# Kernel tuning notes

Hardware: AMD Instinct MI355X
Metric: run time of the kernel (lower is better)

Reference implementation:

```python
import jax, jax.numpy as jnp
import numpy as np

B, S, W = 16, 512, 5
H, E, V = 512, 256, 100000


def setup_inputs() -> dict:
    key = jax.random.key(0)
    ks = jax.random.split(key, 20)
    inp = {
        "hiddens": jax.random.normal(ks[0], (B, S, H), jnp.float32),
        "masks": jax.random.randint(ks[1], (B, S), 0, 2, jnp.int32),
        "begins": jax.random.randint(ks[2], (B, S, W), 0, V, jnp.int32),
        "begin_lens": jax.random.randint(ks[3], (B, S), 0, W + 1, jnp.int32),
        "middles": jax.random.randint(ks[4], (B, S, W), 0, V, jnp.int32),
        "middle_lens": jax.random.randint(ks[5], (B, S), 0, W + 1, jnp.int32),
        "ends": jax.random.randint(ks[6], (B, S, W), 0, V, jnp.int32),
        "end_lens": jax.random.randint(ks[7], (B, S), 0, W + 1, jnp.int32),
        # parameters
        "emb": jax.random.normal(ks[8], (V, E), jnp.float32) * 0.02,
        "W_hidden": jax.random.normal(ks[9], (H, 3 * H), jnp.float32) * (1.0 / np.sqrt(H)),
        "b_hidden": jnp.zeros((3 * H,), jnp.float32),
        "W_begin": jax.random.normal(ks[10], (E, 2 * H), jnp.float32) * (1.0 / np.sqrt(E)),
        "b_begin": jnp.zeros((2 * H,), jnp.float32),
        "W_middle": jax.random.normal(ks[11], (E, 2 * H), jnp.float32) * (1.0 / np.sqrt(E)),
        "b_middle": jnp.zeros((2 * H,), jnp.float32),
        "W_end": jax.random.normal(ks[12], (E, 2 * H), jnp.float32) * (1.0 / np.sqrt(E)),
        "b_end": jnp.zeros((2 * H,), jnp.float32),
        "W_gate": jax.random.normal(ks[13], (H, 9), jnp.float32) * (1.0 / np.sqrt(H)),
        "b_gate": jnp.zeros((9,), jnp.float32),
    }
    return inp


def _len_mask(lens, w):
    # True where the lattice candidate is valid (mimics _make_mask's 1s)
    return jnp.arange(w)[None, None, :] < lens[:, :, None]


def _gates(hiddens, masks, W_gate, b_gate):
    b, s, _ = hiddens.shape
    lmr = hiddens @ W_gate + b_gate                      # (B,S,9)
    left, mid, right = jnp.split(lmr, 3, axis=-1)        # each (B,S,3)
    g = jax.nn.sigmoid(left[:, :-2] + mid[:, 1:-1] + right[:, 2:])  # (B,S-2,3)
    ones = jnp.ones((b, 1), g.dtype)
    zeros = jnp.zeros((b, 1), g.dtype)
    begin_g = jnp.concatenate([ones, g[..., 0], ones], axis=1)
    mid_g = jnp.concatenate([zeros, g[..., 1], zeros], axis=1)
    end_g = jnp.concatenate([ones, g[..., 2], ones], axis=1)
    pad = masks == 0
    z = jnp.zeros((), g.dtype)
    return (jnp.where(pad, z, begin_g), jnp.where(pad, z, mid_g), jnp.where(pad, z, end_g))


def reference(hiddens, masks, begins, begin_lens, middles, middle_lens, ends, end_lens,
              emb, W_hidden, b_hidden, W_begin, b_begin, W_middle, b_middle,
              W_end, b_end, W_gate, b_gate):
    w = begins.shape[-1]
    begin_m = _len_mask(begin_lens, w)
    middle_m = _len_mask(middle_lens, w)
    end_m = _len_mask(end_lens, w)

    begin_kv = emb[begins] @ W_begin + b_begin           # (B,S,W,2H)
    middle_kv = emb[middles] @ W_middle + b_middle
    end_kv = emb[ends] @ W_end + b_end

    query, hidden_key, hidden_value = jnp.split(hiddens @ W_hidden + b_hidden, 3, axis=-1)
    bg, mg, eg = _gates(hiddens, masks, W_gate, b_gate)
    begin_kv = bg[:, :, None, None] * begin_kv
    middle_kv = mg[:, :, None, None] * middle_kv
    end_kv = eg[:, :, None, None] * end_kv

    kv = jnp.concatenate([begin_kv, middle_kv, end_kv], axis=-2)   # (B,S,3W,2H)
    h = hiddens.shape[-1]
    keys, values = jnp.split(kv, 2, axis=-1)
    keys = jnp.concatenate([hidden_key[:, :, None, :], keys], axis=-2)     # (B,S,1+3W,H)
    values = jnp.concatenate([hidden_value[:, :, None, :], values], axis=-2)

    # combined mask: True entries get -1e10 (faithful to masked_fill_(masks, -1e10))
    score_mask = jnp.concatenate(
        [(masks != 0)[:, :, None], begin_m, middle_m, end_m], axis=-1)     # (B,S,1+3W)

    scores = jnp.einsum("bsh,bskh->bsk", query, keys)
    scores = jnp.where(score_mask, jnp.asarray(-1e10, scores.dtype), scores)
    weights = jax.nn.softmax(scores, axis=-1)
    return jnp.einsum("bsk,bskh->bsh", weights, values)
```

## Files before the change

### kernel.cpp

```cpp
#include <hip/hip_runtime.h>
#include <cstdint>
#include <cstddef>


typedef unsigned short u16;
typedef _Float16 f16;
typedef __attribute__((ext_vector_type(8))) f16 f16x8;
typedef __attribute__((ext_vector_type(4))) float f32x4;

#define MROWS 8192
#define SS 512

static __device__ __forceinline__ u16 f2h(float x) {
  f16 h = (f16)x;
  return __builtin_bit_cast(u16, h);
}
static __device__ __forceinline__ float h2f(u16 h) {
  return (float)__builtin_bit_cast(f16, h);
}
static __device__ __forceinline__ float sigm(float x) { return 1.f / (1.f + __expf(-x)); }

static __device__ __forceinline__ void gl2lds(const u16* g, u16* l) {
  __builtin_amdgcn_global_load_lds(
      (const __attribute__((address_space(1))) unsigned int*)g,
      (__attribute__((address_space(3))) unsigned int*)l, 16, 0, 0);
}

__global__ __launch_bounds__(256) void prep_all(
    const float* __restrict__ X, const float* __restrict__ Wg,
    const float* __restrict__ bg, const float* __restrict__ Wh,
    const float* __restrict__ Wb, const float* __restrict__ Wm,
    const float* __restrict__ We, const float* __restrict__ bb,
    const float* __restrict__ bm, const float* __restrict__ be,
    const float* __restrict__ bh, const int* __restrict__ masks,
    u16* __restrict__ Xh, float* __restrict__ lmr, float* __restrict__ s0,
    u16* __restrict__ Breg, u16* __restrict__ Acat, u16* __restrict__ Whq,
    u16* __restrict__ WvT, float* __restrict__ bcat, float* __restrict__ u,
    float* __restrict__ cbuf, int* __restrict__ idx, int* __restrict__ perm,
    int* __restrict__ cnts) {
  __shared__ float shmem[4608];
#define TI(r, c) shmem[(r)*65 + (c)]
  const int b = blockIdx.x;
  const int t = threadIdx.x;
  if (b < 64) {
    int k0 = (b & 7) * 64;
    int n0 = (b >> 3) * 64;
#pragma unroll
    for (int i = 0; i < 16; i++) {
      int li = i * 256 + t; int r = li >> 6, c = li & 63;
      TI(r, c) = Wh[(size_t)(k0 + r) * 1536 + 1024 + n0 + c];
    }
    __syncthreads();
#pragma unroll
    for (int i = 0; i < 16; i++) {
      int li = i * 256 + t; int r = li >> 6, c = li & 63;
      Breg[(size_t)(512 + n0 + r) * 512 + k0 + c] = f2h(TI(c, r));
    }
  } else if (b < 128) {
#pragma unroll
    for (int i = 0; i < 4; i++) {
      int q4 = (b - 64) * 1024 + t * 4 + i;
      int k = q4 >> 7;
      int c4 = (q4 & 127) * 4;
      float4 vq = *(const float4*)(Wh + (size_t)k * 1536 + c4);
      float4 vk = *(const float4*)(Wh + (size_t)k * 1536 + 512 + c4);
      ushort4 qh, kh;
      qh.x = f2h(vq.x); qh.y = f2h(vq.y); qh.z = f2h(vq.z); qh.w = f2h(vq.w);
      kh.x = f2h(vk.x); kh.y = f2h(vk.y); kh.z = f2h(vk.z); kh.w = f2h(vk.w);
      size_t o = (size_t)k * 512 + c4;
      *(ushort4*)(Whq + o) = qh;
      *(ushort4*)(Acat + o) = kh;
    }
  } else if (b < 576) {
    int tid = (b - 128) * 256 + t;
    int n = tid >> 7;
    int kq = (tid & 127) * 4;
    float4 v;
    if (n < 768) {
      int ty = n >> 8, c = n & 255;
      const float* src = (ty == 0 ? Wb : ty == 1 ? Wm : We) + (size_t)c * 1024 + kq;
      v = *(const float4*)src;
    } else if (n < 771) {
      int ty = n - 768;
      const float* src = (ty == 0 ? bb : ty == 1 ? bm : be) + kq;
      v = *(const float4*)src;
    } else {
      v = make_float4(0.f, 0.f, 0.f, 0.f);
    }
    ushort4 h; h.x = f2h(v.x); h.y = f2h(v.y); h.z = f2h(v.z); h.w = f2h(v.w);
    ((ushort4*)(Acat + (size_t)512 * 512))[tid] = h;
  } else if (b < 672) {
    int idx2 = b - 576;
    int ty = idx2 >> 5;
    int rem = idx2 & 31;
    int c0 = (rem & 3) * 64;
    int n0 = (rem >> 2) * 64;
    const float* Wsrc = ty == 0 ? Wb : ty == 1 ? Wm : We;
#pragma unroll
    for (int i = 0; i < 16; i++) {
      int li = i * 256 + t; int r = li >> 6, c = li & 63;
      TI(r, c) = Wsrc[(size_t)(c0 + r) * 1024 + 512 + n0 + c];
    }
    __syncthreads();
#pragma unroll
    for (int i = 0; i < 16; i++) {
      int li = i * 256 + t; int r = li >> 6, c = li & 63;
      WvT[(size_t)(n0 + r) * 768 + ty * 256 + c0 + c] = f2h(TI(c, r));
    }
  } else if (b < 1028) {
    const int lane = t & 63;
    const int widx = (b - 672) * 4 + (t >> 6);
    const int c = lane * 8;
    if (widx < 896) {
      int n = widx;
      float acc = 0.f;
      if (n < 771) {
        const float* src;
        if (n < 768) {
          int ty = n >> 8, ce = n & 255;
          src = (ty == 0 ? Wb : ty == 1 ? Wm : We) + (size_t)ce * 1024 + c;
        } else {
          int ty = n - 768;
          src = (ty == 0 ? bb : ty == 1 ? bm : be) + c;
        }
        float4 a0 = *(const float4*)src;
        float4 a1 = *(const float4*)(src + 4);
        float4 b0 = *(const float4*)(bh + c);
        float4 b1 = *(const float4*)(bh + c + 4);
        acc = a0.x * b0.x + a0.y * b0.y + a0.z * b0.z + a0.w * b0.w +
              a1.x * b1.x + a1.y * b1.y + a1.z * b1.z + a1.w * b1.w;
      }
#pragma unroll
      for (int o = 32; o > 0; o >>= 1) acc += __shfl_xor(acc, o);
      if (lane == 0) bcat[512 + n] = acc;
    } else if (widx < 1408) {
      int k = widx - 896;
      const float* wr = Wh + (size_t)k * 1536;
      float4 a0 = *(const float4*)(wr + c);
      float4 a1 = *(const float4*)(wr + c + 4);
      float4 a2 = *(const float4*)(wr + 512 + c);
      float4 a3 = *(const float4*)(wr + 512 + c + 4);
      float4 b0 = *(const float4*)(bh + 512 + c);
      float4 b1 = *(const float4*)(bh + 512 + c + 4);
      float4 b2 = *(const float4*)(bh + c);
      float4 b3 = *(const float4*)(bh + c + 4);
      float acc = a0.x * b0.x + a0.y * b0.y + a0.z * b0.z + a0.w * b0.w +
                  a1.x * b1.x + a1.y * b1.y + a1.z * b1.z + a1.w * b1.w +
                  a2.x * b2.x + a2.y * b2.y + a2.z * b2.z + a2.w * b2.w +
                  a3.x * b3.x + a3.y * b3.y + a3.z * b3.z + a3.w * b3.w;
#pragma unroll
      for (int o = 32; o > 0; o >>= 1) acc += __shfl_xor(acc, o);
      if (lane == 0) u[k] = acc;
    } else if (widx == 1408) {
      float4 b0 = *(const float4*)(bh + c);
      float4 b1 = *(const float4*)(bh + c + 4);
      float4 b2 = *(const float4*)(bh + 512 + c);
      float4 b3 = *(const float4*)(bh + 512 + c + 4);
      float acc = b0.x * b2.x + b0.y * b2.y + b0.z * b2.z + b0.w * b2.w +
                  b1.x * b3.x + b1.y * b3.y + b1.z * b3.z + b1.w * b3.w;
#pragma unroll
      for (int o = 32; o > 0; o >>= 1) acc += __shfl_xor(acc, o);
      if (lane == 0) cbuf[0] = acc;
    } else if (widx < 1417) {
      int i = (widx - 1409) * 64 + lane;
      bcat[i] = bh[1024 + i];
    }
  } else if (b < 1540) {
    const int xb = b - 1028;
    if (xb < 32) s0[xb * 256 + t] = 0.f;
    for (int i = t; i < 4608; i += 256) shmem[i] = Wg[i];
    __syncthreads();
    const int lane = t & 63, wid = t >> 6;
#pragma unroll
    for (int it = 0; it < 4; it++) {
      int pos = xb * 16 + it * 4 + wid;
      const float* x = X + (size_t)pos * 512 + lane * 8;
      float4 x0 = *(const float4*)x;
      float4 x1 = *(const float4*)(x + 4);
      float xs[8] = {x0.x, x0.y, x0.z, x0.w, x1.x, x1.y, x1.z, x1.w};
      ushort4 h0, h1;
      h0.x = f2h(xs[0]); h0.y = f2h(xs[1]); h0.z = f2h(xs[2]); h0.w = f2h(xs[3]);
      h1.x = f2h(xs[4]); h1.y = f2h(xs[5]); h1.z = f2h(xs[6]); h1.w = f2h(xs[7]);
      ((ushort4*)Xh)[pos * 128 + lane * 2] = h0;
      ((ushort4*)Xh)[pos * 128 + lane * 2 + 1] = h1;
      float p[9];
#pragma unroll
      for (int c = 0; c < 9; c++) p[c] = 0.f;
      const float* wrow = shmem + (lane * 8) * 9;
#pragma unroll
      for (int j = 0; j < 8; j++)
#pragma unroll
        for (int c = 0; c < 9; c++) p[c] += xs[j] * wrow[j * 9 + c];
#pragma unroll
      for (int c = 0; c < 9; c++)
#pragma unroll
        for (int o = 32; o > 0; o >>= 1) p[c] += __shfl_xor(p[c], o);
      if (lane == 0) {
#pragma unroll
        for (int c = 0; c < 9; c++) lmr[(size_t)pos * 9 + c] = p[c] + bg[c];
      }
    }
  } else {
    const int lane = t & 63;
    const int pos = (b - 1540) * 256 + t;
    bool is0 = masks[pos] == 0;
    unsigned long long bal = __ballot(is0);
    unsigned long long below = (lane == 0) ? 0ull : (~0ull >> (64 - lane));
    int rank0 = __popcll(bal & below);
    int rank1 = __popcll((~bal) & below);
    int n0w = __popcll(bal);
    int base0 = 0, base1 = 0;
    if (lane == 0) {
      base0 = atomicAdd(&cnts[0], n0w);
      base1 = atomicAdd(&cnts[1], 64 - n0w);
    }
    base0 = __shfl(base0, 0);
    base1 = __shfl(base1, 0);
    int slot = is0 ? (base0 + rank0) : (8191 - (base1 + rank1));
    perm[pos] = slot;
    idx[slot] = pos;
  }
#undef TI
}

template <int MODE>
__global__ __launch_bounds__(256) void gemm_k(
    const u16* __restrict__ A, const u16* __restrict__ Bt,
    const float* __restrict__ ubias, const float* __restrict__ bcat,
    float* __restrict__ Cf, u16* __restrict__ Cb, int Kdim,
    const u16* __restrict__ Xh, float* __restrict__ s0c,
    const int* __restrict__ idx, const int* __restrict__ cnts,
    const float4* __restrict__ sc4, const u16* __restrict__ HPb,
    const float* __restrict__ bb, const float* __restrict__ bm,
    const float* __restrict__ be) {
  constexpr int BROWS = (MODE == 2) ? 64 : 128;
  constexpr int NT = (MODE == 2) ? 2 : 4;
  __shared__ __align__(16) u16 As[2 * 128 * 32];
  __shared__ __align__(16) u16 Bs[2 * BROWS * 32];

  const int t = threadIdx.x;
  const int lane = t & 63;
  const int wid = t >> 6;
  const int m0 = blockIdx.x * 128;
  const int n0 = blockIdx.y * BROWS;

  bool remap = false;
  if constexpr (MODE == 0) {
    const int cnt0 = cnts[0];
    if (blockIdx.y < 4) {
      if (m0 >= cnt0) return;
      remap = true;
    } else if (blockIdx.y >= 8) {
      if (m0 + 128 <= cnt0) return;
      remap = true;
    }
  }

  int ra0 = m0 + (t >> 2), ra1 = m0 + 64 + (t >> 2);
  if (MODE == 0 && remap) { ra0 = idx[ra0]; ra1 = idx[ra1]; }
  const int rb0 = n0 + (t >> 2), rb1 = n0 + 64 + (t >> 2);
  const int koff = (t & 3) * 8;
  const int lds0 = (t >> 2) * 32 + koff;
  const int lds1 = 2048 + lds0;

  const int wm = (wid & 1) * 64;
  const int wn = (wid >> 1) * (NT * 16);
  const int fr = lane & 15;
  const int kq = (lane >> 4) * 8;

  f32x4 acc[4][NT];
#pragma unroll
  for (int i = 0; i < 4; i++)
#pragma unroll
    for (int j = 0; j < NT; j++) acc[i][j] = (f32x4){0.f, 0.f, 0.f, 0.f};

  auto STAGE = [&](int kb, int buf) {
    gl2lds(&A[(size_t)ra0 * Kdim + kb], &As[buf * 4096 + lds0]);
    gl2lds(&A[(size_t)ra1 * Kdim + kb], &As[buf * 4096 + lds1]);
    gl2lds(&Bt[(size_t)rb0 * Kdim + kb], &Bs[buf * (BROWS * 32) + lds0]);
    if constexpr (BROWS == 128)
      gl2lds(&Bt[(size_t)rb1 * Kdim + kb], &Bs[buf * (BROWS * 32) + lds1]);
  };
  auto COMPUTE = [&](int buf) {
    f16x8 av[4], bv[NT];
#pragma unroll
    for (int i = 0; i < 4; i++)
      av[i] = *(const f16x8*)&As[buf * 4096 + (wm + i * 16 + fr) * 32 + kq];
#pragma unroll
    for (int j = 0; j < NT; j++)
      bv[j] = *(const f16x8*)&Bs[buf * (BROWS * 32) + (wn + j * 16 + fr) * 32 + kq];
#pragma unroll
    for (int mt = 0; mt < 4; mt++)
#pragma unroll
      for (int nt = 0; nt < NT; nt++)
        acc[mt][nt] = __builtin_amdgcn_mfma_f32_16x16x32_f16(
            av[mt], bv[nt], acc[mt][nt], 0, 0, 0);
  };

  STAGE(koff, 0);
  __syncthreads();
  const int nk = Kdim >> 5;
  int buf = 0;
  for (int ki = 0; ki < nk - 1; ++ki) {
    STAGE((ki + 1) * 32 + koff, buf ^ 1);
    COMPUTE(buf);
    __syncthreads();
    buf ^= 1;
  }
  COMPUTE(buf);

  const int r0 = (lane >> 4) * 4;
  if constexpr (MODE == 0) {
    if (blockIdx.y < 4) {
      float pl[4][4];
      int xrow[4][4];
#pragma unroll
      for (int mt = 0; mt < 4; mt++)
#pragma unroll
        for (int r = 0; r < 4; r++) {
          pl[mt][r] = 0.f;
          xrow[mt][r] = idx[m0 + wm + mt * 16 + r0 + r];
        }
#pragma unroll
      for (int mt = 0; mt < 4; mt++)
#pragma unroll
        for (int nt = 0; nt < 4; nt++) {
          int col = n0 + wn + nt * 16 + fr;
          float bv2 = ubias[col];
#pragma unroll
          for (int r = 0; r < 4; r++)
            pl[mt][r] += (acc[mt][nt][r] + bv2) *
                         h2f(Xh[(size_t)xrow[mt][r] * 512 + col]);
        }
#pragma unroll
      for (int mt = 0; mt < 4; mt++)
#pragma unroll
        for (int r = 0; r < 4; r++) {
          float p = pl[mt][r];
          p += __shfl_xor(p, 1);
          p += __shfl_xor(p, 2);
          p += __shfl_xor(p, 4);
          p += __shfl_xor(p, 8);
          if (fr == r) {
            int slot = m0 + wm + mt * 16 + r0 + r;
            atomicAdd(&s0c[slot], p);
          }
        }
      return;
    }
    if (blockIdx.y < 8) {
#pragma unroll
      for (int mt = 0; mt < 4; mt++)
#pragma unroll
        for (int nt = 0; nt < 4; nt++) {
          int col = n0 - 512 + wn + nt * 16 + fr;
          float bv2 = bcat[col];
#pragma unroll
          for (int r = 0; r < 4; r++) {
            int row = m0 + wm + mt * 16 + r0 + r;
            Cb[(size_t)row * 1408 + col] = f2h(acc[mt][nt][r] + bv2);
          }
        }
    } else {
#pragma unroll
      for (int mt = 0; mt < 4; mt++)
#pragma unroll
        for (int nt = 0; nt < 4; nt++) {
          int pcol = n0 - 1024 + wn + nt * 16 + fr;
          float bv2 = bcat[512 + pcol];
#pragma unroll
          for (int r = 0; r < 4; r++) {
            int slot = m0 + wm + mt * 16 + r0 + r;
            Cb[(size_t)slot * 1408 + 512 + pcol] = f2h(acc[mt][nt][r] + bv2);
          }
        }
    }
  } else if constexpr (MODE == 1) {
#pragma unroll
    for (int mt = 0; mt < 4; mt++)
#pragma unroll
      for (int nt = 0; nt < 4; nt++) {
        int col = n0 + wn + nt * 16 + fr;
#pragma unroll
        for (int r = 0; r < 4; r++) {
          int row = m0 + wm + mt * 16 + r0 + r;
          int orow = row < 512 ? row : row + 512;
          Cb[(size_t)orow * 512 + col] = f2h(acc[mt][nt][r]);
        }
      }
  } else {
#pragma unroll
    for (int mt = 0; mt < 4; mt++)
#pragma unroll
      for (int nt = 0; nt < NT; nt++) {
        int col = n0 + wn + nt * 16 + fr;
        float b0 = bb[512 + col];
        float b1 = bm[512 + col];
        float b2 = be[512 + col];
#pragma unroll
        for (int r = 0; r < 4; r++) {
          int row = m0 + wm + mt * 16 + r0 + r;
          float4 s = sc4[row];
          float hv = h2f(HPb[(size_t)row * 1408 + col]);
          Cf[(size_t)row * 512 + col] =
              s.x * hv + s.y * b0 + s.z * b1 + s.w * b2 + acc[mt][nt][r];
        }
      }
  }
}

__global__ __launch_bounds__(256) void attn_kernel(
    const int* __restrict__ masks, const int* __restrict__ begins,
    const int* __restrict__ blens, const int* __restrict__ middles,
    const int* __restrict__ mlens, const int* __restrict__ ends,
    const int* __restrict__ elens, const float* __restrict__ emb,
    const u16* __restrict__ HPb, const float* __restrict__ lmr,
    const float* __restrict__ s0buf, const float* __restrict__ cbuf,
    const int* __restrict__ perm, float4* __restrict__ sc4,
    u16* __restrict__ Ebar) {
  const int t = threadIdx.x;
  const int lane = t & 63;
  const int wid = t >> 6;
  const int pos = blockIdx.x * 4 + wid;
  const int mask = masks[pos];
  const int slot = perm[pos];
  u16* erow = Ebar + (size_t)pos * 768;

  int l0 = min(blens[pos], 5), l1 = min(mlens[pos], 5), l2 = min(elens[pos], 5);
  int nv = l0 + l1 + l2;

  if (mask == 0) {
    float s0 = s0buf[slot] + cbuf[0];
    int ninv = 15 - nv;
    float w0;
    if (ninv == 0) {
      w0 = 1.f;
    } else {
      float Mx = fmaxf(s0, 0.f);
      float e0 = __expf(s0 - Mx);
      w0 = e0 / (e0 + (float)ninv * __expf(-Mx));
    }
    if (lane == 0) sc4[pos] = make_float4(w0, 0.f, 0.f, 0.f);
    ushort4 zz; zz.x = zz.y = zz.z = zz.w = 0;
    *(ushort4*)(erow + 0 * 256 + lane * 4) = zz;
    *(ushort4*)(erow + 1 * 256 + lane * 4) = zz;
    *(ushort4*)(erow + 2 * 256 + lane * 4) = zz;
  } else {
    const int s = pos & (SS - 1);
    float g[3];
    if (s == 0 || s == SS - 1) {
      g[0] = 1.f; g[1] = 0.f; g[2] = 1.f;
    } else {
      const float* p0 = lmr + (size_t)(pos - 1) * 9;
      const float* p1 = lmr + (size_t)pos * 9;
      const float* p2 = lmr + (size_t)(pos + 1) * 9;
      g[0] = sigm(p0[0] + p1[3] + p2[6]);
      g[1] = sigm(p0[1] + p1[4] + p2[7]);
      g[2] = sigm(p0[2] + p1[5] + p2[8]);
    }
    const bool deg = (nv == 15);
    int l[3] = {l0, l1, l2};
    if (deg) { l[0] = 0; l[1] = 0; l[2] = 0; }

    float4 Pt[3];
    float qb[3];
    if (!deg) {
      const u16* prow = HPb + (size_t)slot * 1408 + 512;
#pragma unroll
      for (int ty = 0; ty < 3; ty++) {
        ushort4 pu = *(const ushort4*)(prow + ty * 256 + lane * 4);
        Pt[ty].x = h2f(pu.x); Pt[ty].y = h2f(pu.y);
        Pt[ty].z = h2f(pu.z); Pt[ty].w = h2f(pu.w);
        qb[ty] = h2f(prow[768 + ty]);
      }
    }
    const int* idxp[3];
    idxp[0] = begins + (size_t)pos * 5;
    idxp[1] = middles + (size_t)pos * 5;
    idxp[2] = ends + (size_t)pos * 5;

    float4 ev[3][5];
    float scv[3][5];
    float Mx = deg ? 0.f : -3.0e38f;
#pragma unroll
    for (int ty = 0; ty < 3; ty++) {
#pragma unroll
      for (int w = 0; w < 5; w++) {
        bool act = (w >= l[ty]);
        if (act) {
          ev[ty][w] = *(const float4*)(emb + (size_t)idxp[ty][w] * 256 + lane * 4);
          float sv = 0.f;
          if (!deg) {
            float4 e = ev[ty][w];
            float d = Pt[ty].x * e.x + Pt[ty].y * e.y + Pt[ty].z * e.z + Pt[ty].w * e.w;
#pragma unroll
            for (int o = 32; o > 0; o >>= 1) d += __shfl_xor(d, o);
            sv = g[ty] * (d + qb[ty]);
          }
          scv[ty][w] = sv;
          Mx = fmaxf(Mx, sv);
        }
      }
    }
    float wts0 = deg ? 1.f : 0.f;
    float zs = wts0;
    float wts[3][5];
#pragma unroll
    for (int ty = 0; ty < 3; ty++)
#pragma unroll
      for (int w = 0; w < 5; w++) {
        bool act = (w >= l[ty]);
        float wv = act ? __expf(scv[ty][w] - Mx) : 0.f;
        wts[ty][w] = wv;
        zs += wv;
      }
    float inv = 1.f / zs;
    float alpha[3];
#pragma unroll
    for (int ty = 0; ty < 3; ty++) {
      float ax = 0.f, ay = 0.f, az = 0.f, aw = 0.f, asum = 0.f;
#pragma unroll
      for (int w = 0; w < 5; w++) {
        if (w >= l[ty]) {
          float wk = wts[ty][w];
          asum += wk;
          ax += wk * ev[ty][w].x;
          ay += wk * ev[ty][w].y;
          az += wk * ev[ty][w].z;
          aw += wk * ev[ty][w].w;
        }
      }
      float sg = g[ty] * inv;
      alpha[ty] = sg * asum;
      ushort4 h;
      h.x = f2h(ax * sg); h.y = f2h(ay * sg); h.z = f2h(az * sg); h.w = f2h(aw * sg);
      *(ushort4*)(erow + ty * 256 + lane * 4) = h;
    }
    if (lane == 0) sc4[pos] = make_float4(wts0 * inv, alpha[0], alpha[1], alpha[2]);
  }
}

extern "C" void kernel_launch(void* const* d_in, const int* in_sizes, int n_in,
                              void* d_out, int out_size, void* d_ws, size_t ws_size,
                              hipStream_t stream) {
  const float* hiddens = (const float*)d_in[0];
  const int* masks = (const int*)d_in[1];
  const int* begins = (const int*)d_in[2];
  const int* blens = (const int*)d_in[3];
  const int* middles = (const int*)d_in[4];
  const int* mlens = (const int*)d_in[5];
  const int* ends = (const int*)d_in[6];
  const int* elens = (const int*)d_in[7];
  const float* emb = (const float*)d_in[8];
  const float* Wh = (const float*)d_in[9];
  const float* bh = (const float*)d_in[10];
  const float* Wb = (const float*)d_in[11];
  const float* bb = (const float*)d_in[12];
  const float* Wm = (const float*)d_in[13];
  const float* bm = (const float*)d_in[14];
  const float* We = (const float*)d_in[15];
  const float* be = (const float*)d_in[16];
  const float* Wg = (const float*)d_in[17];
  const float* bg = (const float*)d_in[18];
  float* out = (float*)d_out;

  char* ws = (char*)d_ws;
  size_t off = 0;
  auto alloc = [&](size_t bytes) -> char* {
    char* p = ws + off;
    off += (bytes + 255) & ~(size_t)255;
    return p;
  };
  u16* Xh = (u16*)alloc((size_t)8192 * 512 * 2);
  u16* Whq = (u16*)alloc((size_t)512 * 512 * 2);
  u16* Acat = (u16*)alloc((size_t)1408 * 512 * 2);
  u16* Breg = (u16*)alloc((size_t)1920 * 512 * 2);
  u16* WvT = (u16*)alloc((size_t)512 * 768 * 2);
  u16* HPb = (u16*)alloc((size_t)8192 * 1408 * 2);
  float* lmr = (float*)alloc((size_t)8192 * 9 * 4);
  float* s0c = (float*)alloc((size_t)8192 * 4);
  float* bcat = (float*)alloc((size_t)1408 * 4);
  float* u = (float*)alloc((size_t)512 * 4);
  float* cbuf = (float*)alloc((size_t)4);
  float* sc4 = (float*)alloc((size_t)8192 * 4 * 4);
  u16* Ebar = (u16*)alloc((size_t)8192 * 768 * 2);
  int* idx = (int*)alloc((size_t)8192 * 4);
  int* perm = (int*)alloc((size_t)8192 * 4);
  int* cnts = (int*)alloc((size_t)256);
  if (off > ws_size) return;

  hipMemsetAsync(cnts, 0, 8, stream);
  prep_all<<<1572, 256, 0, stream>>>(hiddens, Wg, bg, Wh, Wb, Wm, We, bb, bm, be,
                                     bh, masks, Xh, lmr, s0c, Breg, Acat, Whq,
                                     WvT, bcat, u, cbuf, idx, perm, cnts);
  gemm_k<1><<<dim3(11, 4), 256, 0, stream>>>(
      Acat, Whq, nullptr, nullptr, nullptr, Breg, 512, nullptr, nullptr,
      nullptr, nullptr, nullptr, nullptr, nullptr, nullptr, nullptr);
  gemm_k<0><<<dim3(64, 15), 256, 0, stream>>>(
      Xh, Breg, u, bcat, nullptr, HPb, 512, Xh, s0c, idx, cnts,
      nullptr, nullptr, nullptr, nullptr, nullptr);
  attn_kernel<<<2048, 256, 0, stream>>>(masks, begins, blens, middles, mlens,
                                        ends, elens, emb, HPb, lmr, s0c, cbuf,
                                        perm, (float4*)sc4, Ebar);
  gemm_k<2><<<dim3(64, 8), 256, 0, stream>>>(
      Ebar, WvT, nullptr, nullptr, out, nullptr, 768, nullptr, nullptr,
      nullptr, nullptr, (const float4*)sc4, HPb, bb, bm, be);
}
```

Measured before the change: 287.7 us.

## Fuse weight-product GEMM into prep kernel, reading fp32 weights directly

```diff
diff --git a/kernel.cpp b/kernel.cpp
--- a/kernel.cpp
+++ b/kernel.cpp
@@ -34,11 +34,13 @@
     const float* __restrict__ bm, const float* __restrict__ be,
     const float* __restrict__ bh, const int* __restrict__ masks,
     u16* __restrict__ Xh, float* __restrict__ lmr, float* __restrict__ s0,
-    u16* __restrict__ Breg, u16* __restrict__ Acat, u16* __restrict__ Whq,
-    u16* __restrict__ WvT, float* __restrict__ bcat, float* __restrict__ u,
-    float* __restrict__ cbuf, int* __restrict__ idx, int* __restrict__ perm,
-    int* __restrict__ cnts) {
-  __shared__ float shmem[4608];
+    u16* __restrict__ Breg, u16* __restrict__ WvT, float* __restrict__ bcat,
+    float* __restrict__ u, float* __restrict__ cbuf, int* __restrict__ idx,
+    int* __restrict__ perm, int* __restrict__ cnts) {
+  __shared__ __align__(16) char smem_raw[32768];
+  float* shmem = (float*)smem_raw;
+  u16* As = (u16*)smem_raw;
+  u16* Bs = (u16*)(smem_raw + 16384);
 #define TI(r, c) shmem[(r)*65 + (c)]
   const int b = blockIdx.x;
   const int t = threadIdx.x;
@@ -56,41 +58,8 @@
       int li = i * 256 + t; int r = li >> 6, c = li & 63;
       Breg[(size_t)(512 + n0 + r) * 512 + k0 + c] = f2h(TI(c, r));
     }
-  } else if (b < 128) {
-#pragma unroll
-    for (int i = 0; i < 4; i++) {
-      int q4 = (b - 64) * 1024 + t * 4 + i;
-      int k = q4 >> 7;
-      int c4 = (q4 & 127) * 4;
-      float4 vq = *(const float4*)(Wh + (size_t)k * 1536 + c4);
-      float4 vk = *(const float4*)(Wh + (size_t)k * 1536 + 512 + c4);
-      ushort4 qh, kh;
-      qh.x = f2h(vq.x); qh.y = f2h(vq.y); qh.z = f2h(vq.z); qh.w = f2h(vq.w);
-      kh.x = f2h(vk.x); kh.y = f2h(vk.y); kh.z = f2h(vk.z); kh.w = f2h(vk.w);
-      size_t o = (size_t)k * 512 + c4;
-      *(ushort4*)(Whq + o) = qh;
-      *(ushort4*)(Acat + o) = kh;
-    }
-  } else if (b < 576) {
-    int tid = (b - 128) * 256 + t;
-    int n = tid >> 7;
-    int kq = (tid & 127) * 4;
-    float4 v;
-    if (n < 768) {
-      int ty = n >> 8, c = n & 255;
-      const float* src = (ty == 0 ? Wb : ty == 1 ? Wm : We) + (size_t)c * 1024 + kq;
-      v = *(const float4*)src;
-    } else if (n < 771) {
-      int ty = n - 768;
-      const float* src = (ty == 0 ? bb : ty == 1 ? bm : be) + kq;
-      v = *(const float4*)src;
-    } else {
-      v = make_float4(0.f, 0.f, 0.f, 0.f);
-    }
-    ushort4 h; h.x = f2h(v.x); h.y = f2h(v.y); h.z = f2h(v.z); h.w = f2h(v.w);
-    ((ushort4*)(Acat + (size_t)512 * 512))[tid] = h;
-  } else if (b < 672) {
-    int idx2 = b - 576;
+  } else if (b < 160) {
+    int idx2 = b - 64;
     int ty = idx2 >> 5;
     int rem = idx2 & 31;
     int c0 = (rem & 3) * 64;
@@ -107,9 +76,9 @@
       int li = i * 256 + t; int r = li >> 6, c = li & 63;
       WvT[(size_t)(n0 + r) * 768 + ty * 256 + c0 + c] = f2h(TI(c, r));
     }
-  } else if (b < 1028) {
+  } else if (b < 516) {
     const int lane = t & 63;
-    const int widx = (b - 672) * 4 + (t >> 6);
+    const int widx = (b - 160) * 4 + (t >> 6);
     const int c = lane * 8;
     if (widx < 896) {
       int n = widx;
@@ -165,8 +134,8 @@
       int i = (widx - 1409) * 64 + lane;
       bcat[i] = bh[1024 + i];
     }
-  } else if (b < 1540) {
-    const int xb = b - 1028;
+  } else if (b < 1028) {
+    const int xb = b - 516;
     if (xb < 32) s0[xb * 256 + t] = 0.f;
     for (int i = t; i < 4608; i += 256) shmem[i] = Wg[i];
     __syncthreads();
@@ -200,9 +169,9 @@
         for (int c = 0; c < 9; c++) lmr[(size_t)pos * 9 + c] = p[c] + bg[c];
       }
     }
-  } else {
+  } else if (b < 1060) {
     const int lane = t & 63;
-    const int pos = (b - 1540) * 256 + t;
+    const int pos = (b - 1028) * 256 + t;
     bool is0 = masks[pos] == 0;
     unsigned long long bal = __ballot(is0);
     unsigned long long below = (lane == 0) ? 0ull : (~0ull >> (64 - lane));
@@ -219,6 +188,96 @@
     int slot = is0 ? (base0 + rank0) : (8191 - (base1 + rank1));
     perm[pos] = slot;
     idx[slot] = pos;
+  } else {
+    const int b2 = b - 1060;
+    const int m0 = (b2 % 11) * 128;
+    const int n0 = (b2 / 11) * 128;
+    const int lane = t & 63;
+    const int wid = t >> 6;
+    const int row = t >> 2;
+    const int koff = (t & 3) * 8;
+    const int lds0 = row * 32 + koff;
+    const int lds1 = 2048 + lds0;
+
+    auto asrc = [&](int r) -> const float* {
+      if (r < 512) return Wh + (size_t)r * 1536 + 512;
+      int n = r - 512;
+      if (n < 768)
+        return (n < 256 ? Wb : n < 512 ? Wm : We) + (size_t)(n & 255) * 1024;
+      if (n < 771) return (n == 768 ? bb : n == 769 ? bm : be);
+      return nullptr;
+    };
+    const float* pa0 = asrc(m0 + row);
+    const float* pa1 = asrc(m0 + 64 + row);
+    const float* pb0 = Wh + (size_t)(n0 + row) * 1536;
+    const float* pb1 = Wh + (size_t)(n0 + 64 + row) * 1536;
+
+    const int wm = (wid & 1) * 64;
+    const int wn = (wid >> 1) * 64;
+    const int fr = lane & 15;
+    const int kq = (lane >> 4) * 8;
+
+    f32x4 acc[4][4];
+#pragma unroll
+    for (int i = 0; i < 4; i++)
+#pragma unroll
+      for (int j = 0; j < 4; j++) acc[i][j] = (f32x4){0.f, 0.f, 0.f, 0.f};
+
+    auto cvt8 = [&](const float* p, int col) -> f16x8 {
+      f16x8 h{};
+      if (p) {
+        float4 v0 = *(const float4*)(p + col);
+        float4 v1 = *(const float4*)(p + col + 4);
+        h[0] = (f16)v0.x; h[1] = (f16)v0.y; h[2] = (f16)v0.z; h[3] = (f16)v0.w;
+        h[4] = (f16)v1.x; h[5] = (f16)v1.y; h[6] = (f16)v1.z; h[7] = (f16)v1.w;
+      }
+      return h;
+    };
+    auto STAGE = [&](int kb, int buf) {
+      *(f16x8*)&As[buf * 4096 + lds0] = cvt8(pa0, kb + koff);
+      *(f16x8*)&As[buf * 4096 + lds1] = cvt8(pa1, kb + koff);
+      *(f16x8*)&Bs[buf * 4096 + lds0] = cvt8(pb0, kb + koff);
+      *(f16x8*)&Bs[buf * 4096 + lds1] = cvt8(pb1, kb + koff);
+    };
+    auto COMPUTE = [&](int buf) {
+      f16x8 av[4], bv[4];
+#pragma unroll
+      for (int i = 0; i < 4; i++) {
+        av[i] = *(const f16x8*)&As[buf * 4096 + (wm + i * 16 + fr) * 32 + kq];
+        bv[i] = *(const f16x8*)&Bs[buf * 4096 + (wn + i * 16 + fr) * 32 + kq];
+      }
+#pragma unroll
+      for (int mt = 0; mt < 4; mt++)
+#pragma unroll
+        for (int nt = 0; nt < 4; nt++)
+          acc[mt][nt] = __builtin_amdgcn_mfma_f32_16x16x32_f16(
+              av[mt], bv[nt], acc[mt][nt], 0, 0, 0);
+    };
+
+    STAGE(0, 0);
+    __syncthreads();
+    int buf = 0;
+    for (int ki = 0; ki < 15; ++ki) {
+      STAGE((ki + 1) * 32, buf ^ 1);
+      COMPUTE(buf);
+      __syncthreads();
+      buf ^= 1;
+    }
+    COMPUTE(buf);
+
+    const int r0 = (lane >> 4) * 4;
+#pragma unroll
+    for (int mt = 0; mt < 4; mt++)
+#pragma unroll
+      for (int nt = 0; nt < 4; nt++) {
+        int col = n0 + wn + nt * 16 + fr;
+#pragma unroll
+        for (int r = 0; r < 4; r++) {
+          int orow0 = m0 + wm + mt * 16 + r0 + r;
+          int orow = orow0 < 512 ? orow0 : orow0 + 512;
+          Breg[(size_t)orow * 512 + col] = f2h(acc[mt][nt][r]);
+        }
+      }
   }
 #undef TI
 }
@@ -375,19 +434,6 @@
           }
         }
     }
-  } else if constexpr (MODE == 1) {
-#pragma unroll
-    for (int mt = 0; mt < 4; mt++)
-#pragma unroll
-      for (int nt = 0; nt < 4; nt++) {
-        int col = n0 + wn + nt * 16 + fr;
-#pragma unroll
-        for (int r = 0; r < 4; r++) {
-          int row = m0 + wm + mt * 16 + r0 + r;
-          int orow = row < 512 ? row : row + 512;
-          Cb[(size_t)orow * 512 + col] = f2h(acc[mt][nt][r]);
-        }
-      }
   } else {
 #pragma unroll
     for (int mt = 0; mt < 4; mt++)
@@ -572,8 +618,6 @@
     return p;
   };
   u16* Xh = (u16*)alloc((size_t)8192 * 512 * 2);
-  u16* Whq = (u16*)alloc((size_t)512 * 512 * 2);
-  u16* Acat = (u16*)alloc((size_t)1408 * 512 * 2);
   u16* Breg = (u16*)alloc((size_t)1920 * 512 * 2);
   u16* WvT = (u16*)alloc((size_t)512 * 768 * 2);
   u16* HPb = (u16*)alloc((size_t)8192 * 1408 * 2);
@@ -590,12 +634,9 @@
   if (off > ws_size) return;
 
   hipMemsetAsync(cnts, 0, 8, stream);
-  prep_all<<<1572, 256, 0, stream>>>(hiddens, Wg, bg, Wh, Wb, Wm, We, bb, bm, be,
-                                     bh, masks, Xh, lmr, s0c, Breg, Acat, Whq,
-                                     WvT, bcat, u, cbuf, idx, perm, cnts);
-  gemm_k<1><<<dim3(11, 4), 256, 0, stream>>>(
-      Acat, Whq, nullptr, nullptr, nullptr, Breg, 512, nullptr, nullptr,
-      nullptr, nullptr, nullptr, nullptr, nullptr, nullptr, nullptr);
+  prep_all<<<1104, 256, 0, stream>>>(hiddens, Wg, bg, Wh, Wb, Wm, We, bb, bm, be,
+                                     bh, masks, Xh, lmr, s0c, Breg, WvT, bcat,
+                                     u, cbuf, idx, perm, cnts);
   gemm_k<0><<<dim3(64, 15), 256, 0, stream>>>(
       Xh, Breg, u, bcat, nullptr, HPb, 512, Xh, s0c, idx, cnts,
       nullptr, nullptr, nullptr, nullptr, nullptr);
```

New measurement: 303.6 us. 5.5% more time.
